# Kernel optimization log

Hardware: AMD Instinct MI355X
Metric: run time of the kernel (lower is better)

## Reference

```python
import jax, jax.numpy as jnp
import numpy as np

N_CG = 50000          # number of coarse-grained beads (residues)
ATOMS_PER_CG = 13     # heavy atoms per residue -> vector channels
N_AT = N_CG * ATOMS_PER_CG
FEAT = 128            # feature_dim
DEG = 16
E = N_CG * DEG
VOCAB = 100           # nn.Embedding(100, feature_dim)


def setup_inputs() -> dict:
    key = jax.random.key(0)
    ks = jax.random.split(key, 6)
    cg_z = jax.random.randint(ks[0], (N_CG,), 1, VOCAB)                 # residue types (0 = padding)
    cg_xyz = jax.random.normal(ks[1], (N_CG, 3), jnp.float32) * 10.0    # CA positions
    src = jnp.repeat(jnp.arange(N_CG), DEG)
    dst = jax.random.randint(ks[2], (E,), 0, N_CG)
    CG_nbr_list = jnp.stack([src, dst], axis=1)                          # [E,2] CG graph edges
    mapping = jnp.repeat(jnp.arange(N_CG), ATOMS_PER_CG)                 # atom -> CG bead (sorted)
    ca_idx = jnp.arange(N_CG) * ATOMS_PER_CG + 1                         # CA atom index per residue
    emb = jax.random.normal(ks[3], (VOCAB, FEAT), jnp.float32) * 0.02
    W_msg = jax.random.normal(ks[4], (FEAT, FEAT), jnp.float32) / np.sqrt(FEAT)
    W_vec = jax.random.normal(ks[5], (FEAT, ATOMS_PER_CG), jnp.float32) / np.sqrt(FEAT)
    return dict(cg_xyz=cg_xyz, emb=emb, W_msg=W_msg, W_vec=W_vec,
                cg_z=cg_z, CG_nbr_list=CG_nbr_list, mapping=mapping, ca_idx=ca_idx)


def reference(cg_xyz, emb, W_msg, W_vec, cg_z, CG_nbr_list, mapping, ca_idx):
    n_cg = cg_xyz.shape[0]
    n_at = mapping.shape[0]
    # embedding with padding_idx=0 (row 0 produces zeros)
    S_I = emb[cg_z] * (cg_z != 0)[:, None].astype(emb.dtype)             # [N_cg, F]
    # --- equivariant conv (PaiNN-like stand-in for self.equivaraintconv) ---
    i, j = CG_nbr_list[:, 0], CG_nbr_list[:, 1]
    r = cg_xyz[j] - cg_xyz[i]                                            # [E,3]
    unit = r / (jnp.linalg.norm(r, axis=-1, keepdims=True) + 1e-8)
    m = jax.nn.silu((S_I[i] + S_I[j]) @ W_msg)                           # [E,F] edge messages
    w = m @ W_vec                                                        # [E,C] per-channel weights
    cg_v = jax.ops.segment_sum(w[:, :, None] * unit[:, None, :], i,
                               num_segments=n_cg)                        # [N_cg, C, 3]
    # --- CG2ChannelIdx: occurrence rank of each atom within its CG group ---
    at = jnp.arange(n_at)
    first = jax.ops.segment_min(at, mapping, num_segments=n_cg)          # start index of each group
    channel = at - first[mapping]                                        # [N_at]
    # --- decode: gather relative vectors, zero the CA offset, add CG position ---
    xyz_rel = cg_v[mapping, channel, :]                                  # [N_at,3]
    xyz_rel = xyz_rel.at[ca_idx].set(0.0)   # xyz_rel[ca_idx] -= clone(xyz_rel[ca_idx])
    xyz_recon = xyz_rel + cg_xyz[mapping]
    return xyz_recon
```

## Files before the change

### kernel.cpp

```cpp
#include <hip/hip_runtime.h>
#include <math.h>

#define N_CG   50000
#define APC    13
#define N_AT   (N_CG * APC)
#define FEAT   128
#define DEG    16
#define VOCAB  100
#define TPAD   16
#define CG_PER_BLK 16
#define ROWS_PER_BLK 16

__global__ void p_kernel(const float* __restrict__ emb,
                         const float* __restrict__ Wmsg,
                         float* __restrict__ P) {
    int z = blockIdx.x;
    int f = threadIdx.x;
    float acc = 0.f;
    #pragma unroll 8
    for (int k = 0; k < FEAT; ++k)
        acc += emb[z * FEAT + k] * Wmsg[k * FEAT + f];
    P[z * FEAT + f] = (z != 0) ? acc : 0.f;
}

__global__ void table_kernel(const float* __restrict__ P,
                             const float* __restrict__ Wvec,
                             float* __restrict__ T) {
    __shared__ float hs[ROWS_PER_BLK][FEAT + 1];
    int t = threadIdx.x;
    int row0 = blockIdx.x * ROWS_PER_BLK;

    #pragma unroll
    for (int i = 0; i < (ROWS_PER_BLK * FEAT) / 256; ++i) {
        int v = t + i * 256;
        int r = v >> 7, f = v & 127;
        int row = row0 + r;
        int zi = row / VOCAB, zj = row % VOCAB;
        float h = P[zi * FEAT + f] + P[zj * FEAT + f];
        hs[r][f] = h / (1.f + expf(-h));
    }
    __syncthreads();

    if (t < ROWS_PER_BLK * APC) {
        int r = t / APC, c = t % APC;
        float s = 0.f;
        #pragma unroll 8
        for (int f = 0; f < FEAT; ++f)
            s += hs[r][f] * Wvec[f * APC + c];
        T[(size_t)(row0 + r) * TPAD + c] = s;
    }
}

__global__ void recon_kernel(const float* __restrict__ xyz,
                             const int*   __restrict__ nbr,
                             const int*   __restrict__ cg_z,
                             const int*   __restrict__ ca_idx,
                             const float* __restrict__ T,
                             float* __restrict__ out) {
    __shared__ float4 eu[CG_PER_BLK][DEG + 1];
    __shared__ int  erow[CG_PER_BLK][DEG + 1];

    int t = threadIdx.x;
    int cg0 = blockIdx.x * CG_PER_BLK;

    {
        int g = t >> 4;
        int k = t & 15;
        int cg = cg0 + g;
        int e = cg * DEG + k;
        int j = nbr[2 * e + 1];
        float xi0 = xyz[cg * 3 + 0];
        float xi1 = xyz[cg * 3 + 1];
        float xi2 = xyz[cg * 3 + 2];
        float dx = xyz[j * 3 + 0] - xi0;
        float dy = xyz[j * 3 + 1] - xi1;
        float dz = xyz[j * 3 + 2] - xi2;
        float inv = 1.f / (sqrtf(dx * dx + dy * dy + dz * dz) + 1e-8f);
        int zi = cg_z[cg];
        int zj = cg_z[j];
        eu[g][k] = make_float4(dx * inv, dy * inv, dz * inv, 0.f);
        erow[g][k] = zi * VOCAB + zj;
    }
    __syncthreads();

    if (t < CG_PER_BLK * APC) {
        int g = t / APC, c = t % APC;
        int cg = cg0 + g;
        float a0 = 0.f, a1 = 0.f, a2 = 0.f;
        #pragma unroll
        for (int k = 0; k < DEG; ++k) {
            float4 u = eu[g][k];
            int row = erow[g][k];
            float w = T[(size_t)row * TPAD + c];
            a0 += w * u.x;
            a1 += w * u.y;
            a2 += w * u.z;
        }
        if (c == 1) { a0 = 0.f; a1 = 0.f; a2 = 0.f; }
        int a = (ca_idx[cg] - 1) + c;
        float xi0 = xyz[cg * 3 + 0];
        float xi1 = xyz[cg * 3 + 1];
        float xi2 = xyz[cg * 3 + 2];
        out[a * 3 + 0] = a0 + xi0;
        out[a * 3 + 1] = a1 + xi1;
        out[a * 3 + 2] = a2 + xi2;
    }
}

extern "C" void kernel_launch(void* const* d_in, const int* in_sizes, int n_in,
                              void* d_out, int out_size, void* d_ws, size_t ws_size,
                              hipStream_t stream) {
    const float* cg_xyz  = (const float*)d_in[0];
    const float* emb     = (const float*)d_in[1];
    const float* W_msg   = (const float*)d_in[2];
    const float* W_vec   = (const float*)d_in[3];
    const int*   cg_z    = (const int*)d_in[4];
    const int*   nbr     = (const int*)d_in[5];
    const int*   ca_idx  = (const int*)d_in[7];
    float* out = (float*)d_out;

    float* P = (float*)d_ws;
    float* T = P + VOCAB * FEAT;

    p_kernel<<<VOCAB, FEAT, 0, stream>>>(emb, W_msg, P);
    table_kernel<<<(VOCAB * VOCAB) / ROWS_PER_BLK, 256, 0, stream>>>(P, W_vec, T);
    recon_kernel<<<N_CG / CG_PER_BLK, 256, 0, stream>>>(
        cg_xyz, nbr, cg_z, ca_idx, T, out);
}
```

Measured before the change: 34.10 us.

## Fuse embedding projection and table build, pack xyz with types, coalesce output stores

Merges the two table-building kernels into one prep kernel in which each block recomputes the emb@W_msg rows it needs, removing a launch and the P round trip. The same launch also packs xyz and cg_z into float4 so the recon kernel fetches position and type with one gather per neighbour. Recon results are staged in shared memory and written out as coalesced float4 stores. In exchange, the projection is recomputed redundantly across table blocks, and the output store assumes contiguous atom ordering per block rather than using ca_idx for the address. The code also contains a dead no-op conditional.

```diff
diff --git a/kernel.cpp b/kernel.cpp
--- a/kernel.cpp
+++ b/kernel.cpp
@@ -3,107 +3,122 @@
 
 #define N_CG   50000
 #define APC    13
-#define N_AT   (N_CG * APC)
 #define FEAT   128
 #define DEG    16
 #define VOCAB  100
 #define TPAD   16
+#define ZJT    16
+#define NTILE  7
+#define TBLK   (VOCAB * NTILE)
+#define PACKB  ((N_CG + 255) / 256)
 #define CG_PER_BLK 16
-#define ROWS_PER_BLK 16
 
-__global__ void p_kernel(const float* __restrict__ emb,
-                         const float* __restrict__ Wmsg,
-                         float* __restrict__ P) {
-    int z = blockIdx.x;
-    int f = threadIdx.x;
-    float acc = 0.f;
-    #pragma unroll 8
-    for (int k = 0; k < FEAT; ++k)
-        acc += emb[z * FEAT + k] * Wmsg[k * FEAT + f];
-    P[z * FEAT + f] = (z != 0) ? acc : 0.f;
-}
+__global__ void prep_kernel(const float* __restrict__ xyz,
+                            const int*   __restrict__ cg_z,
+                            const float* __restrict__ emb,
+                            const float* __restrict__ Wmsg,
+                            const float* __restrict__ Wvec,
+                            float*  __restrict__ T,
+                            float4* __restrict__ xyz4) {
+    int b = blockIdx.x;
+    int t = threadIdx.x;
+    if (b >= TBLK) {
+        int i = (b - TBLK) * 256 + t;
+        if (i < N_CG)
+            xyz4[i] = make_float4(xyz[3*i], xyz[3*i+1], xyz[3*i+2],
+                                  __int_as_float(cg_z[i]));
+        return;
+    }
+    __shared__ float Pl[ZJT + 1][FEAT];
+    __shared__ float hs[ZJT][FEAT + 1];
 
-__global__ void table_kernel(const float* __restrict__ P,
-                             const float* __restrict__ Wvec,
-                             float* __restrict__ T) {
-    __shared__ float hs[ROWS_PER_BLK][FEAT + 1];
-    int t = threadIdx.x;
-    int row0 = blockIdx.x * ROWS_PER_BLK;
+    int zi    = b / NTILE;
+    int zj0   = (b % NTILE) * ZJT;
+    int nrows = (VOCAB - zj0 < ZJT) ? (VOCAB - zj0) : ZJT;
 
-    #pragma unroll
-    for (int i = 0; i < (ROWS_PER_BLK * FEAT) / 256; ++i) {
-        int v = t + i * 256;
-        int r = v >> 7, f = v & 127;
-        int row = row0 + r;
-        int zi = row / VOCAB, zj = row % VOCAB;
-        float h = P[zi * FEAT + f] + P[zj * FEAT + f];
+    int ntask = (nrows + 1) * FEAT;
+    for (int i = t; i < ntask; i += 256) {
+        int r = i >> 7, f = i & 127;
+        int z = (r == nrows) ? zi : (zj0 + r);
+        float acc = 0.f;
+        if (z != 0) {
+            #pragma unroll 8
+            for (int k = 0; k < FEAT; ++k)
+                acc += emb[z * FEAT + k] * Wmsg[k * FEAT + f];
+        }
+        Pl[r][f] = acc;
+    }
+    __syncthreads();
+
+    for (int i = t; i < nrows * FEAT; i += 256) {
+        int r = i >> 7, f = i & 127;
+        float h = Pl[nrows][f] + Pl[r][f];
         hs[r][f] = h / (1.f + expf(-h));
     }
     __syncthreads();
 
-    if (t < ROWS_PER_BLK * APC) {
+    if (t < nrows * APC) {
         int r = t / APC, c = t % APC;
         float s = 0.f;
         #pragma unroll 8
         for (int f = 0; f < FEAT; ++f)
             s += hs[r][f] * Wvec[f * APC + c];
-        T[(size_t)(row0 + r) * TPAD + c] = s;
+        T[(size_t)(zi * VOCAB + zj0 + r) * TPAD + c] = s;
     }
 }
 
-__global__ void recon_kernel(const float* __restrict__ xyz,
-                             const int*   __restrict__ nbr,
-                             const int*   __restrict__ cg_z,
-                             const int*   __restrict__ ca_idx,
-                             const float* __restrict__ T,
+__global__ void recon_kernel(const float4* __restrict__ xyz4,
+                             const int*    __restrict__ nbr,
+                             const int*    __restrict__ ca_idx,
+                             const float*  __restrict__ T,
                              float* __restrict__ out) {
     __shared__ float4 eu[CG_PER_BLK][DEG + 1];
-    __shared__ int  erow[CG_PER_BLK][DEG + 1];
+    __shared__ float4 xis[CG_PER_BLK];
+    __shared__ float  obuf[CG_PER_BLK * APC * 3];
 
     int t = threadIdx.x;
     int cg0 = blockIdx.x * CG_PER_BLK;
 
     {
-        int g = t >> 4;
-        int k = t & 15;
+        int g = t >> 4, k = t & 15;
         int cg = cg0 + g;
-        int e = cg * DEG + k;
-        int j = nbr[2 * e + 1];
-        float xi0 = xyz[cg * 3 + 0];
-        float xi1 = xyz[cg * 3 + 1];
-        float xi2 = xyz[cg * 3 + 2];
-        float dx = xyz[j * 3 + 0] - xi0;
-        float dy = xyz[j * 3 + 1] - xi1;
-        float dz = xyz[j * 3 + 2] - xi2;
-        float inv = 1.f / (sqrtf(dx * dx + dy * dy + dz * dz) + 1e-8f);
-        int zi = cg_z[cg];
-        int zj = cg_z[j];
-        eu[g][k] = make_float4(dx * inv, dy * inv, dz * inv, 0.f);
-        erow[g][k] = zi * VOCAB + zj;
+        int e  = cg * DEG + k;
+        int j  = nbr[2 * e + 1];
+        float4 pj = xyz4[j];
+        float4 pi = xyz4[cg];
+        if (k == 0) xis[g] = pi;
+        float dx = pj.x - pi.x, dy = pj.y - pi.y, dz = pj.z - pi.z;
+        float inv = 1.f / (sqrtf(dx*dx + dy*dy + dz*dz) + 1e-8f);
+        int row = __float_as_int(pi.w) * VOCAB + __float_as_int(pj.w);
+        eu[g][k] = make_float4(dx*inv, dy*inv, dz*inv, __int_as_float(row));
     }
     __syncthreads();
 
     if (t < CG_PER_BLK * APC) {
         int g = t / APC, c = t % APC;
-        int cg = cg0 + g;
         float a0 = 0.f, a1 = 0.f, a2 = 0.f;
         #pragma unroll
         for (int k = 0; k < DEG; ++k) {
             float4 u = eu[g][k];
-            int row = erow[g][k];
+            int row = __float_as_int(u.w);
             float w = T[(size_t)row * TPAD + c];
-            a0 += w * u.x;
-            a1 += w * u.y;
-            a2 += w * u.z;
+            a0 += w * u.x; a1 += w * u.y; a2 += w * u.z;
         }
-        if (c == 1) { a0 = 0.f; a1 = 0.f; a2 = 0.f; }
-        int a = (ca_idx[cg] - 1) + c;
-        float xi0 = xyz[cg * 3 + 0];
-        float xi1 = xyz[cg * 3 + 1];
-        float xi2 = xyz[cg * 3 + 2];
-        out[a * 3 + 0] = a0 + xi0;
-        out[a * 3 + 1] = a1 + xi1;
-        out[a * 3 + 2] = a2 + xi2;
+        int cg = cg0 + g;
+        int czero = ca_idx[cg] - (cg * APC + 1);
+        if (c == czero + 1 - 1 + 1 - 1 + (ca_idx[cg] - cg * APC - 1) * 0 &&
+            c == ca_idx[cg] - cg * APC) { }
+        if (c == ca_idx[cg] - cg * APC) { a0 = 0.f; a1 = 0.f; a2 = 0.f; }
+        float4 xi = xis[g];
+        obuf[t * 3 + 0] = a0 + xi.x;
+        obuf[t * 3 + 1] = a1 + xi.y;
+        obuf[t * 3 + 2] = a2 + xi.z;
+    }
+    __syncthreads();
+
+    if (t < (CG_PER_BLK * APC * 3) / 4) {
+        float4* ov = (float4*)(out + (size_t)blockIdx.x * (CG_PER_BLK * APC * 3));
+        ov[t] = ((const float4*)obuf)[t];
     }
 }
 
@@ -119,11 +134,11 @@
     const int*   ca_idx  = (const int*)d_in[7];
     float* out = (float*)d_out;
 
-    float* P = (float*)d_ws;
-    float* T = P + VOCAB * FEAT;
+    float*  T    = (float*)d_ws;
+    float4* xyz4 = (float4*)((char*)d_ws + (size_t)VOCAB * VOCAB * TPAD * 4);
 
-    p_kernel<<<VOCAB, FEAT, 0, stream>>>(emb, W_msg, P);
-    table_kernel<<<(VOCAB * VOCAB) / ROWS_PER_BLK, 256, 0, stream>>>(P, W_vec, T);
+    prep_kernel<<<TBLK + PACKB, 256, 0, stream>>>(
+        cg_xyz, cg_z, emb, W_msg, W_vec, T, xyz4);
     recon_kernel<<<N_CG / CG_PER_BLK, 256, 0, stream>>>(
-        cg_xyz, nbr, cg_z, ca_idx, T, out);
+        xyz4, nbr, ca_idx, T, out);
 }
```

Measured after the change: 73.66 us. 116% more time.
